# Kernel tuning notes

Measured on AMD Instinct MI355X. Metric: run time of the kernel, lower is better.

Reference implementation:

```python
import jax, jax.numpy as jnp
import numpy as np

T_LEN, BATCH, HID = 1024, 8, 1024
TEMP = 0.1
EPS = 1e-12  # torch F.normalize eps


def setup_inputs() -> dict:
    key = jax.random.key(0)
    k1, k2, k3, k4 = jax.random.split(key, 4)
    h1 = jax.random.normal(k1, (T_LEN, BATCH, HID), jnp.float32)
    h2 = jax.random.normal(k2, (T_LEN, BATCH, HID), jnp.float32)
    # learned params of nn.Sequential(Linear, ReLU, Linear, ReLU)
    W1 = jax.random.normal(k3, (HID, HID), jnp.float32) * 0.02
    b1 = jnp.zeros((HID,), jnp.float32)
    W2 = jax.random.normal(k4, (HID, HID), jnp.float32) * 0.02
    b2 = jnp.zeros((HID,), jnp.float32)
    return {"h1": h1, "h2": h2, "W1": W1, "b1": b1, "W2": W2, "b2": b2}


def _mlp(x, W1, b1, W2, b2):
    x = jax.nn.relu(x @ W1 + b1)
    return jax.nn.relu(x @ W2 + b2)


def _info_nce(emb_i, emb_j, temperature=TEMP):
    # emb_i, emb_j: [n, h] with n = 2*(t-1)
    n = emb_i.shape[0]
    z_i = emb_i / jnp.maximum(jnp.linalg.norm(emb_i, axis=1, keepdims=True), EPS)
    z_j = emb_j / jnp.maximum(jnp.linalg.norm(emb_j, axis=1, keepdims=True), EPS)
    reps = jnp.concatenate([z_i, z_j], axis=0)          # [2n, h]
    sim = reps @ reps.T                                  # cosine sim (rows are unit)
    logits = sim / temperature
    exp_l = jnp.exp(logits)
    # denominator excludes self-similarity (scatter of 0 at position i)
    denom = exp_l.sum(axis=1) - jnp.diagonal(exp_l)      # [2n]
    log_denom = jnp.log(denom)
    idx = jnp.arange(n)
    l_ab = -logits[idx, idx + n] + log_denom[:n]         # l(k, k+N)
    l_ba = -logits[idx + n, idx] + log_denom[n:]         # l(k+N, k)
    return (l_ab.sum() + l_ba.sum()) / (2.0 * n)


def reference(h1, h2, W1, b1, W2, b2):
    h1 = jnp.transpose(h1, (1, 0, 2))  # [b, t, h]
    h2 = jnp.transpose(h2, (1, 0, 2))
    h1 = _mlp(h1, W1, b1, W2, b2)
    h2 = _mlp(h2, W1, b1, W2, b2)
    h_t_1 = jnp.concatenate([h1[:, 1:, :], h2[:, 1:, :]], axis=1)    # [b, 2(t-1), h]
    h_t_2 = jnp.concatenate([h1[:, :-1, :], h2[:, :-1, :]], axis=1)
    # original loop overwrites cl_loss each iteration -> only last batch row counts
    cl_loss = _info_nce(h_t_1[-1], h_t_2[-1])
    return (h1, h2, cl_loss)
```

## Files before the change

### kernel.cpp

```cpp
#include <hip/hip_runtime.h>
#include <cstdint>
#include <cstddef>

using u16 = unsigned short;
using u8  = unsigned char;
typedef short short8 __attribute__((ext_vector_type(8)));
typedef __bf16 bf16x8 __attribute__((ext_vector_type(8)));
typedef float f32x4 __attribute__((ext_vector_type(4)));
typedef u16 u16x4 __attribute__((ext_vector_type(4)));
typedef int i32x4 __attribute__((ext_vector_type(4)));
typedef int i32x8 __attribute__((ext_vector_type(8)));

__device__ __forceinline__ u16 f2bf(float f) {
  union { float f; uint32_t u; } v; v.f = f;
  uint32_t r = v.u + 0x7FFF + ((v.u >> 16) & 1);
  return (u16)(r >> 16);
}
__device__ __forceinline__ float bf2f(u16 b) {
  union { uint32_t u; float f; } v; v.u = ((uint32_t)b) << 16;
  return v.f;
}
__device__ __forceinline__ u8 f2fp8(float f) {
  return (u8)(__builtin_amdgcn_cvt_pk_fp8_f32(f, f, 0, 0) & 0xFF);
}

__device__ __forceinline__ void gload16(const void* g, void* l) {
  __builtin_amdgcn_global_load_lds(
      (const __attribute__((address_space(1))) void*)g,
      (__attribute__((address_space(3))) void*)l, 16, 0, 0);
}

#define MFMAQ8(M0, N0, AF, BF)                                             \
  {                                                                        \
    _Pragma("unroll") for (int m_ = 0; m_ < 4; ++m_) {                     \
      _Pragma("unroll") for (int n_ = 0; n_ < 2; ++n_) {                   \
        acc[(M0) + m_][(N0) + n_] =                                        \
            __builtin_amdgcn_mfma_scale_f32_16x16x128_f8f6f4(              \
                AF[m_], BF[n_], acc[(M0) + m_][(N0) + n_],                 \
                0, 0, 0, 127, 0, 127);                                     \
      }                                                                    \
    }                                                                      \
  }

template <int EPI>
__global__ __launch_bounds__(512, 2) void gemm_fp8(
    const u8* __restrict__ A, const u8* __restrict__ Bt,
    const float* __restrict__ bias,
    u8* __restrict__ C8, float* __restrict__ Cf)
{
  constexpr int Kb = 1024, N = 1024, NT = 8;
  __shared__ alignas(16) u8 lds[131072];

  const int t = (int)threadIdx.x;
  const int lane = t & 63, wid = t >> 6;
  const int wr = wid >> 2, wc = wid & 3;
  const int li = lane & 15, hk = lane >> 4;

  const int orig = (int)blockIdx.x;
  const int cpx = (int)gridDim.x >> 3;
  const int swz = (orig & 7) * cpx + (orig >> 3);
  const int bm = swz >> 2, bn = swz & 3;
  const int arow0 = bm * 256, brow0 = bn * 256;

  const int Rl = lane >> 3;
  const int sc16 = ((lane & 7) ^ Rl) << 4;
  const int wid2 = wid * 2;

  const int c0b = (((hk << 1) + 0) ^ (li & 7)) << 4;
  const int c1b = (((hk << 1) + 1) ^ (li & 7)) << 4;

  f32x4 acc[8][4];
#pragma unroll
  for (int m = 0; m < 8; ++m)
#pragma unroll
    for (int n = 0; n < 4; ++n)
#pragma unroll
      for (int j = 0; j < 4; ++j) acc[m][n][j] = 0.0f;

  auto STAGE = [&](const u8* G, int growbase, int tau, int ldsoff) {
#pragma unroll
    for (int l = 0; l < 2; ++l) {
      const u8* g = G + (size_t)(growbase + (wid2 + l) * 8 + Rl) * Kb +
                    tau * 128 + sc16;
      gload16(g, lds + ldsoff + (wid2 + l) * 1024);
    }
  };
  auto RD = [&](const u8* base, int row) -> i32x8 {
    const u8* p = base + row * 128;
    i32x4 lo = *reinterpret_cast<const i32x4*>(p + c0b);
    i32x4 hi = *reinterpret_cast<const i32x4*>(p + c1b);
    i32x8 r;
    r[0] = lo[0]; r[1] = lo[1]; r[2] = lo[2]; r[3] = lo[3];
    r[4] = hi[0]; r[5] = hi[1]; r[6] = hi[2]; r[7] = hi[3];
    return r;
  };

  i32x8 aa[4], bb01[2], bb23[2];

  STAGE(Bt, brow0 + 0,   0, 65536 + 0);
  STAGE(Bt, brow0 + 128, 0, 65536 + 16384);
  STAGE(A,  arow0 + 0,   0, 0);
  STAGE(A,  arow0 + 128, 0, 16384);
  STAGE(Bt, brow0 + 0,   1, 65536 + 32768);
  STAGE(Bt, brow0 + 128, 1, 65536 + 32768 + 16384);
  STAGE(A,  arow0 + 0,   1, 32768);
  STAGE(A,  arow0 + 128, 1, 32768 + 16384);
  asm volatile("s_waitcnt vmcnt(8)" ::: "memory");
  __builtin_amdgcn_s_barrier();

  {
    const u8* Ab0 = lds + wr * 16384;
    const u8* Bb0 = lds + 65536 + wc * 8192;
#pragma unroll
    for (int m = 0; m < 4; ++m) aa[m] = RD(Ab0, m * 16 + li);
#pragma unroll
    for (int n = 0; n < 2; ++n) bb01[n] = RD(Bb0, n * 16 + li);
  }

  for (int tau = 0; tau < NT; ++tau) {
    const int cur = tau & 1, nxt = cur ^ 1;
    const u8* Ab  = lds + cur * 32768 + wr * 16384;
    const u8* Bb  = lds + 65536 + cur * 32768 + wc * 8192;
    const u8* Abn = lds + nxt * 32768 + wr * 16384;
    const u8* Bbn = lds + 65536 + nxt * 32768 + wc * 8192;

#pragma unroll
    for (int n = 0; n < 2; ++n) bb23[n] = RD(Bb, 32 + n * 16 + li);
    asm volatile("s_waitcnt lgkmcnt(4)" ::: "memory");
    __builtin_amdgcn_sched_barrier(0);
    __builtin_amdgcn_s_setprio(1);
    MFMAQ8(0, 0, aa, bb01);
    __builtin_amdgcn_s_setprio(0);

    asm volatile("s_waitcnt lgkmcnt(0)" ::: "memory");
    __builtin_amdgcn_sched_barrier(0);
    __builtin_amdgcn_s_setprio(1);
    MFMAQ8(0, 2, aa, bb23);
    __builtin_amdgcn_s_setprio(0);
    __builtin_amdgcn_sched_barrier(0);
#pragma unroll
    for (int m = 0; m < 4; ++m) aa[m] = RD(Ab, (m + 4) * 16 + li);
    __builtin_amdgcn_s_barrier();

    if (tau + 2 < NT) {
      STAGE(Bt, brow0 + 0,   tau + 2, 65536 + cur * 32768);
      STAGE(Bt, brow0 + 128, tau + 2, 65536 + cur * 32768 + 16384);
    }
    asm volatile("s_waitcnt lgkmcnt(0)" ::: "memory");
    __builtin_amdgcn_sched_barrier(0);
    __builtin_amdgcn_s_setprio(1);
    MFMAQ8(4, 2, aa, bb23);
    __builtin_amdgcn_s_setprio(0);
    __builtin_amdgcn_s_barrier();

    if (tau + 2 < NT) {
      STAGE(A, arow0 + 0,   tau + 2, cur * 32768);
      STAGE(A, arow0 + 128, tau + 2, cur * 32768 + 16384);
      asm volatile("s_waitcnt vmcnt(8)" ::: "memory");
    } else if (tau + 1 < NT) {
      asm volatile("s_waitcnt vmcnt(0)" ::: "memory");
    }
    __builtin_amdgcn_s_barrier();
    __builtin_amdgcn_s_setprio(1);
    MFMAQ8(4, 0, aa, bb01);
    __builtin_amdgcn_s_setprio(0);
    __builtin_amdgcn_sched_barrier(0);
    if (tau + 1 < NT) {
#pragma unroll
      for (int m = 0; m < 4; ++m) aa[m] = RD(Abn, m * 16 + li);
#pragma unroll
      for (int n = 0; n < 2; ++n) bb01[n] = RD(Bbn, n * 16 + li);
    }
  }

#pragma unroll
  for (int m = 0; m < 8; ++m) {
#pragma unroll
    for (int n = 0; n < 4; ++n) {
      const int gcol = brow0 + wc * 64 + n * 16 + li;
      const float bv = bias[gcol];
#pragma unroll
      for (int j = 0; j < 4; ++j) {
        const int grow = arow0 + wr * 128 + m * 16 + hk * 4 + j;
        float v = fmaxf(acc[m][n][j] * 0.001953125f + bv, 0.0f);
        if (EPI == 0) {
          C8[(size_t)grow * N + gcol] = f2fp8(v * 8.0f);
        } else {
          int tensor = grow >> 13, rr = grow & 8191;
          int tt = rr >> 3, b_ = rr & 7;
          Cf[(size_t)tensor * 8388608 + (size_t)b_ * 1048576 +
             (size_t)tt * 1024 + gcol] = v;
        }
      }
    }
  }
}

__device__ __forceinline__ void gemm_core_128(
    const u16* __restrict__ A, const u16* __restrict__ B,
    int arow0, int brow0, int K,
    u16* As, u16* Bs, f32x4 (&acc)[4][4])
{
  const int t = (int)threadIdx.x;
  const int lane = t & 63, wv = t >> 6;
  const int wr = wv >> 1, wc = wv & 1;
  const int li = lane & 15, hk = lane >> 4;
  const int sr = t >> 3, sc = t & 7;

#pragma unroll
  for (int m = 0; m < 4; ++m)
#pragma unroll
    for (int n = 0; n < 4; ++n)
#pragma unroll
      for (int j = 0; j < 4; ++j) acc[m][n][j] = 0.0f;

  for (int kt = 0; kt < K; kt += 64) {
#pragma unroll
    for (int i = 0; i < 4; ++i) {
      int row = i * 32 + sr;
      int coff = (sc ^ (row & 7)) << 3;
      const u16* ga = A + (size_t)(arow0 + row) * K + kt + coff;
      const u16* gb = B + (size_t)(brow0 + row) * K + kt + coff;
      u16* la = As + i * 2048 + wv * 512;
      u16* lb = Bs + i * 2048 + wv * 512;
      gload16(ga, la);
      gload16(gb, lb);
    }
    __syncthreads();
#pragma unroll
    for (int kk = 0; kk < 2; ++kk) {
      short8 av[4], bv[4];
#pragma unroll
      for (int m = 0; m < 4; ++m) {
        int ra = wr * 64 + m * 16 + li;
        int ca = ((kk << 2) + hk) ^ (ra & 7);
        av[m] = *reinterpret_cast<const short8*>(As + ra * 64 + ca * 8);
      }
#pragma unroll
      for (int n = 0; n < 4; ++n) {
        int rb = wc * 64 + n * 16 + li;
        int cb = ((kk << 2) + hk) ^ (rb & 7);
        bv[n] = *reinterpret_cast<const short8*>(Bs + rb * 64 + cb * 8);
      }
#pragma unroll
      for (int m = 0; m < 4; ++m)
#pragma unroll
        for (int n = 0; n < 4; ++n)
          acc[m][n] = __builtin_amdgcn_mfma_f32_16x16x32_bf16(
              __builtin_bit_cast(bf16x8, av[m]),
              __builtin_bit_cast(bf16x8, bv[n]),
              acc[m][n], 0, 0, 0);
    }
    __syncthreads();
  }
}

__global__ void prep_kernel(const float* __restrict__ h1,
                            const float* __restrict__ h2,
                            const float* __restrict__ W1,
                            const float* __restrict__ W2,
                            u8* __restrict__ X8,
                            u8* __restrict__ W1t,
                            u8* __restrict__ W2t,
                            float* __restrict__ S)
{
  __shared__ float tile[32][33];
  int bid = (int)blockIdx.x;
  if (bid < 16384) {
    size_t i4 = ((size_t)bid * 256 + threadIdx.x) * 4;
    const float* src = (i4 < 8388608) ? (h1 + i4) : (h2 + (i4 - 8388608));
    float4 v = *reinterpret_cast<const float4*>(src);
    int lo = __builtin_amdgcn_cvt_pk_fp8_f32(v.x * 8.0f, v.y * 8.0f, 0, 0);
    int all4 = __builtin_amdgcn_cvt_pk_fp8_f32(v.z * 8.0f, v.w * 8.0f, lo, 1);
    *reinterpret_cast<uint32_t*>(X8 + i4) = (uint32_t)all4;
    return;
  }
  bid -= 16384;
  const float* W;
  u8* Wt;
  if (bid < 1024) {
    W = W1; Wt = W1t;
  } else if (bid < 2048) {
    W = W2; Wt = W2t; bid -= 1024;
  } else {
    for (int i = (int)threadIdx.x; i < 2064; i += 256) S[i] = 0.0f;
    return;
  }
  const int bx = bid & 31, by = bid >> 5;
  const int tx = (int)threadIdx.x & 31, ty = (int)threadIdx.x >> 5;
#pragma unroll
  for (int i = 0; i < 4; ++i)
    tile[ty + i * 8][tx] = W[(size_t)(by * 32 + ty + i * 8) * 1024 + bx * 32 + tx];
  __syncthreads();
#pragma unroll
  for (int i = 0; i < 4; ++i)
    Wt[(size_t)(bx * 32 + ty + i * 8) * 1024 + by * 32 + tx] =
        f2fp8(tile[tx][ty + i * 8] * 64.0f);
}

__global__ __launch_bounds__(256) void sim_kernel(const u16* __restrict__ Z,
                                                  float* __restrict__ S,
                                                  float* __restrict__ dots)
{
  __shared__ alignas(16) u16 As[128 * 64];
  __shared__ alignas(16) u16 Bs[128 * 64];
  if ((int)blockIdx.x >= 256) {
    const int wv4 = ((int)blockIdx.x - 256) * 4 + ((int)threadIdx.x >> 6);
    const int lane = (int)threadIdx.x & 63;
    float s = 0.0f;
    for (int wid = wv4; wid < 2046; wid += 128) {
      int tensor = wid / 1023, tl = wid % 1023 + 1;
      const u16* ra = Z + ((size_t)tensor * 1024 + tl) * 1024;
      const u16* rb = ra - 1024;
#pragma unroll
      for (int i = 0; i < 2; ++i) {
        short8 a = *reinterpret_cast<const short8*>(ra + lane * 16 + i * 8);
        short8 b = *reinterpret_cast<const short8*>(rb + lane * 16 + i * 8);
#pragma unroll
        for (int j = 0; j < 8; ++j) s += bf2f((u16)a[j]) * bf2f((u16)b[j]);
      }
    }
#pragma unroll
    for (int d = 1; d < 64; d <<= 1) s += __shfl_xor(s, d);
    if (lane == 0) atomicAdd(dots, s);
    return;
  }
  const int bm = (int)blockIdx.x / 16, bn = (int)blockIdx.x % 16;
  f32x4 acc[4][4];
  gemm_core_128(Z, Z, bm * 128, bn * 128, 1024, As, Bs, acc);

  const int t = (int)threadIdx.x;
  const int lane = t & 63, wv = t >> 6;
  const int wr = wv >> 1, wc = wv & 1;
  const int li = lane & 15, hk = lane >> 4;

#pragma unroll
  for (int m = 0; m < 4; ++m) {
#pragma unroll
    for (int j = 0; j < 4; ++j) {
      int grow = bm * 128 + wr * 64 + m * 16 + hk * 4 + j;
      float s = 0.0f;
#pragma unroll
      for (int n = 0; n < 4; ++n) {
        int gcol = bn * 128 + wc * 64 + n * 16 + li;
        float logit = (grow == gcol) ? 10.0f : acc[m][n][j] * 10.0f;
        float w = (gcol == 0 || gcol == 1023 || gcol == 1024 || gcol == 2047)
                      ? 1.0f : 2.0f;
        s += w * expf(logit);
      }
      s += __shfl_xor(s, 1); s += __shfl_xor(s, 2);
      s += __shfl_xor(s, 4); s += __shfl_xor(s, 8);
      if (li == 0) atomicAdd(&S[grow], s);
    }
  }
}

__global__ void row_normalize(const float* __restrict__ out, u16* __restrict__ Z)
{
  const int row = (int)blockIdx.x;
  const int t = (int)threadIdx.x;
  const float* src = out + ((row < 1024)
      ? ((size_t)7 * 1048576 + (size_t)row * 1024)
      : ((size_t)8388608 + (size_t)7 * 1048576 + (size_t)(row - 1024) * 1024));
  float4 v = reinterpret_cast<const float4*>(src)[t];
  float ss = v.x * v.x + v.y * v.y + v.z * v.z + v.w * v.w;
#pragma unroll
  for (int d = 1; d < 64; d <<= 1) ss += __shfl_xor(ss, d);
  __shared__ float red[4];
  if ((t & 63) == 0) red[t >> 6] = ss;
  __syncthreads();
  float tot = red[0] + red[1] + red[2] + red[3];
  float inv = 1.0f / fmaxf(sqrtf(tot), 1e-12f);
  u16x4 o;
  o[0] = f2bf(v.x * inv); o[1] = f2bf(v.y * inv);
  o[2] = f2bf(v.z * inv); o[3] = f2bf(v.w * inv);
  reinterpret_cast<u16x4*>(Z + (size_t)row * 1024)[t] = o;
}

__global__ void finalize_kernel(const float* __restrict__ S,
                                const float* __restrict__ dots,
                                float* __restrict__ out_loss)
{
  const int t = (int)threadIdx.x;
  float acc = 0.0f;
  for (int i = t; i < 2048; i += 256) {
    int tl = i & 1023;
    float w = (tl == 0 || tl == 1023) ? 1.0f : 2.0f;
    acc += w * logf(S[i] - 22026.465794806718f);
  }
  __shared__ float red[256];
  red[t] = acc;
  __syncthreads();
  for (int s2 = 128; s2 > 0; s2 >>= 1) {
    if (t < s2) red[t] += red[t + s2];
    __syncthreads();
  }
  if (t == 0) out_loss[0] = (red[0] - 20.0f * dots[0]) / 4092.0f;
}

extern "C" void kernel_launch(void* const* d_in, const int* in_sizes, int n_in,
                              void* d_out, int out_size, void* d_ws, size_t ws_size,
                              hipStream_t stream)
{
  const float* h1 = (const float*)d_in[0];
  const float* h2 = (const float*)d_in[1];
  const float* W1 = (const float*)d_in[2];
  const float* b1 = (const float*)d_in[3];
  const float* W2 = (const float*)d_in[4];
  const float* b2 = (const float*)d_in[5];
  float* out = (float*)d_out;

  char* ws = (char*)d_ws;
  u8*    X8   = (u8*)ws;
  u8*    Y18  = (u8*)(ws + 16777216);
  u8*    W1t  = (u8*)(ws + 33554432);
  u8*    W2t  = (u8*)(ws + 34603008);
  u16*   Zb   = (u16*)(ws + 35651584);
  float* S    = (float*)(ws + 39845888);
  float* dots = S + 2048;

  prep_kernel<<<18433, 256, 0, stream>>>(h1, h2, W1, W2, X8, W1t, W2t, S);

  gemm_fp8<0><<<256, 512, 0, stream>>>(X8, W1t, b1, Y18, nullptr);
  gemm_fp8<1><<<256, 512, 0, stream>>>(Y18, W2t, b2, nullptr, out);

  row_normalize<<<2048, 256, 0, stream>>>(out, Zb);
  sim_kernel<<<288, 256, 0, stream>>>(Zb, S, dots);
  finalize_kernel<<<1, 256, 0, stream>>>(S, dots, out + 16777216);
}
```

Baseline: 95.76 us.

## Shrink similarity GEMM tiles to 64x64 and fold positive-pair dots into epilogue

The similarity kernel moves from 128x128 tiles on 256 blocks to 64x64 tiles on 1024 blocks, so more blocks cover the GPU's compute units. The separate 32 extra blocks that recomputed adjacent-row dot products from Z are removed. Those dots are now taken from the GEMM accumulators at the superdiagonal inside the epilogue. In exchange, smaller tiles reuse less data per load, so total global/LDS traffic rises, and there are more atomics on S.

```diff
diff --git a/kernel.cpp b/kernel.cpp
--- a/kernel.cpp
+++ b/kernel.cpp
@@ -196,56 +196,58 @@
   }
 }
 
-__device__ __forceinline__ void gemm_core_128(
-    const u16* __restrict__ A, const u16* __restrict__ B,
-    int arow0, int brow0, int K,
-    u16* As, u16* Bs, f32x4 (&acc)[4][4])
-{
+__global__ __launch_bounds__(256) void sim_kernel(const u16* __restrict__ Z,
+                                                  float* __restrict__ S,
+                                                  float* __restrict__ dots)
+{
+  __shared__ alignas(16) u16 As[64 * 64];
+  __shared__ alignas(16) u16 Bs[64 * 64];
   const int t = (int)threadIdx.x;
   const int lane = t & 63, wv = t >> 6;
   const int wr = wv >> 1, wc = wv & 1;
   const int li = lane & 15, hk = lane >> 4;
   const int sr = t >> 3, sc = t & 7;
-
-#pragma unroll
-  for (int m = 0; m < 4; ++m)
-#pragma unroll
-    for (int n = 0; n < 4; ++n)
+  const int bm = (int)blockIdx.x >> 5, bn = (int)blockIdx.x & 31;
+  const int arow0 = bm * 64, brow0 = bn * 64;
+
+  f32x4 acc[2][2];
+#pragma unroll
+  for (int m = 0; m < 2; ++m)
+#pragma unroll
+    for (int n = 0; n < 2; ++n)
 #pragma unroll
       for (int j = 0; j < 4; ++j) acc[m][n][j] = 0.0f;
 
-  for (int kt = 0; kt < K; kt += 64) {
-#pragma unroll
-    for (int i = 0; i < 4; ++i) {
-      int row = i * 32 + sr;
+  for (int kt = 0; kt < 1024; kt += 64) {
+#pragma unroll
+    for (int l = 0; l < 2; ++l) {
+      int row = l * 32 + sr;
       int coff = (sc ^ (row & 7)) << 3;
-      const u16* ga = A + (size_t)(arow0 + row) * K + kt + coff;
-      const u16* gb = B + (size_t)(brow0 + row) * K + kt + coff;
-      u16* la = As + i * 2048 + wv * 512;
-      u16* lb = Bs + i * 2048 + wv * 512;
-      gload16(ga, la);
-      gload16(gb, lb);
+      const u16* ga = Z + (size_t)(arow0 + row) * 1024 + kt + coff;
+      const u16* gb = Z + (size_t)(brow0 + row) * 1024 + kt + coff;
+      gload16(ga, As + l * 2048 + wv * 512);
+      gload16(gb, Bs + l * 2048 + wv * 512);
     }
     __syncthreads();
 #pragma unroll
     for (int kk = 0; kk < 2; ++kk) {
-      short8 av[4], bv[4];
-#pragma unroll
-      for (int m = 0; m < 4; ++m) {
-        int ra = wr * 64 + m * 16 + li;
+      short8 av[2], bv[2];
+#pragma unroll
+      for (int m = 0; m < 2; ++m) {
+        int ra = wr * 32 + m * 16 + li;
         int ca = ((kk << 2) + hk) ^ (ra & 7);
         av[m] = *reinterpret_cast<const short8*>(As + ra * 64 + ca * 8);
       }
 #pragma unroll
-      for (int n = 0; n < 4; ++n) {
-        int rb = wc * 64 + n * 16 + li;
+      for (int n = 0; n < 2; ++n) {
+        int rb = wc * 32 + n * 16 + li;
         int cb = ((kk << 2) + hk) ^ (rb & 7);
         bv[n] = *reinterpret_cast<const short8*>(Bs + rb * 64 + cb * 8);
       }
 #pragma unroll
-      for (int m = 0; m < 4; ++m)
-#pragma unroll
-        for (int n = 0; n < 4; ++n)
+      for (int m = 0; m < 2; ++m)
+#pragma unroll
+        for (int n = 0; n < 2; ++n)
           acc[m][n] = __builtin_amdgcn_mfma_f32_16x16x32_bf16(
               __builtin_bit_cast(bf16x8, av[m]),
               __builtin_bit_cast(bf16x8, bv[n]),
@@ -253,6 +255,32 @@
     }
     __syncthreads();
   }
+
+  float dsum = 0.0f;
+#pragma unroll
+  for (int m = 0; m < 2; ++m) {
+#pragma unroll
+    for (int j = 0; j < 4; ++j) {
+      int grow = arow0 + wr * 32 + m * 16 + hk * 4 + j;
+      float s = 0.0f;
+#pragma unroll
+      for (int n = 0; n < 2; ++n) {
+        int gcol = brow0 + wc * 32 + n * 16 + li;
+        float g = acc[m][n][j];
+        float logit = (grow == gcol) ? 10.0f : g * 10.0f;
+        float w = (gcol == 0 || gcol == 1023 || gcol == 1024 || gcol == 2047)
+                      ? 1.0f : 2.0f;
+        s += w * expf(logit);
+        if (gcol == grow + 1 && (grow & 1023) != 1023) dsum += g;
+      }
+      s += __shfl_xor(s, 1); s += __shfl_xor(s, 2);
+      s += __shfl_xor(s, 4); s += __shfl_xor(s, 8);
+      if (li == 0) atomicAdd(&S[grow], s);
+    }
+  }
+#pragma unroll
+  for (int d = 1; d < 64; d <<= 1) dsum += __shfl_xor(dsum, d);
+  if (lane == 0) atomicAdd(dots, dsum);
 }
 
 __global__ void prep_kernel(const float* __restrict__ h1,
@@ -298,63 +326,6 @@
         f2fp8(tile[tx][ty + i * 8] * 64.0f);
 }
 
-__global__ __launch_bounds__(256) void sim_kernel(const u16* __restrict__ Z,
-                                                  float* __restrict__ S,
-                                                  float* __restrict__ dots)
-{
-  __shared__ alignas(16) u16 As[128 * 64];
-  __shared__ alignas(16) u16 Bs[128 * 64];
-  if ((int)blockIdx.x >= 256) {
-    const int wv4 = ((int)blockIdx.x - 256) * 4 + ((int)threadIdx.x >> 6);
-    const int lane = (int)threadIdx.x & 63;
-    float s = 0.0f;
-    for (int wid = wv4; wid < 2046; wid += 128) {
-      int tensor = wid / 1023, tl = wid % 1023 + 1;
-      const u16* ra = Z + ((size_t)tensor * 1024 + tl) * 1024;
-      const u16* rb = ra - 1024;
-#pragma unroll
-      for (int i = 0; i < 2; ++i) {
-        short8 a = *reinterpret_cast<const short8*>(ra + lane * 16 + i * 8);
-        short8 b = *reinterpret_cast<const short8*>(rb + lane * 16 + i * 8);
-#pragma unroll
-        for (int j = 0; j < 8; ++j) s += bf2f((u16)a[j]) * bf2f((u16)b[j]);
-      }
-    }
-#pragma unroll
-    for (int d = 1; d < 64; d <<= 1) s += __shfl_xor(s, d);
-    if (lane == 0) atomicAdd(dots, s);
-    return;
-  }
-  const int bm = (int)blockIdx.x / 16, bn = (int)blockIdx.x % 16;
-  f32x4 acc[4][4];
-  gemm_core_128(Z, Z, bm * 128, bn * 128, 1024, As, Bs, acc);
-
-  const int t = (int)threadIdx.x;
-  const int lane = t & 63, wv = t >> 6;
-  const int wr = wv >> 1, wc = wv & 1;
-  const int li = lane & 15, hk = lane >> 4;
-
-#pragma unroll
-  for (int m = 0; m < 4; ++m) {
-#pragma unroll
-    for (int j = 0; j < 4; ++j) {
-      int grow = bm * 128 + wr * 64 + m * 16 + hk * 4 + j;
-      float s = 0.0f;
-#pragma unroll
-      for (int n = 0; n < 4; ++n) {
-        int gcol = bn * 128 + wc * 64 + n * 16 + li;
-        float logit = (grow == gcol) ? 10.0f : acc[m][n][j] * 10.0f;
-        float w = (gcol == 0 || gcol == 1023 || gcol == 1024 || gcol == 2047)
-                      ? 1.0f : 2.0f;
-        s += w * expf(logit);
-      }
-      s += __shfl_xor(s, 1); s += __shfl_xor(s, 2);
-      s += __shfl_xor(s, 4); s += __shfl_xor(s, 8);
-      if (li == 0) atomicAdd(&S[grow], s);
-    }
-  }
-}
-
 __global__ void row_normalize(const float* __restrict__ out, u16* __restrict__ Z)
 {
   const int row = (int)blockIdx.x;
@@ -425,6 +396,6 @@
   gemm_fp8<1><<<256, 512, 0, stream>>>(Y18, W2t, b2, nullptr, out);
 
   row_normalize<<<2048, 256, 0, stream>>>(out, Zb);
-  sim_kernel<<<288, 256, 0, stream>>>(Zb, S, dots);
+  sim_kernel<<<1024, 256, 0, stream>>>(Zb, S, dots);
   finalize_kernel<<<1, 256, 0, stream>>>(S, dots, out + 16777216);
 }
```

Measured after the change: 138.2 us. 1.44x slower.
